# Performance work log

Hardware: AMD Instinct MI355X
Metric: run time of the kernel (lower is better)

## Reference

```python
import jax, jax.numpy as jnp
import numpy as np
import math

B, N, D_FEAT, D_POS, L, H, DK, DV, DM, DI, M = 16, 512, 3, 3, 4, 8, 64, 64, 512, 2048, 64


def _ln(x, g, b, eps=1e-6):
    mu = jnp.mean(x, axis=-1, keepdims=True)
    var = jnp.mean((x - mu) ** 2, axis=-1, keepdims=True)
    return (x - mu) / jnp.sqrt(var + eps) * g + b


def _gelu(x):  # erf-form gelu, matching the torch source exactly
    return x * 0.5 * (1.0 + jax.lax.erf(x / math.sqrt(2.0)))


def setup_inputs() -> dict:
    keys = iter(jax.random.split(jax.random.key(0), 48))
    r = lambda *s: jax.random.normal(next(keys), s, jnp.float32) * 0.02
    inp = {
        'feat_seq': jax.random.normal(next(keys), (B, N, D_FEAT), jnp.float32),
        'r_pos_mat': jax.random.normal(next(keys), (B, N, N, D_POS), jnp.float32),
        'masked_pos': jax.random.randint(next(keys), (B, M), 0, N),
        'fe_w1': r(D_FEAT, DM), 'fe_b1': jnp.zeros((DM,), jnp.float32),
        'fe_w2': r(DM, DM), 'fe_b2': jnp.zeros((DM,), jnp.float32),
        'wq': r(L, DM, H * DK), 'bq': jnp.zeros((L, H * DK), jnp.float32),
        'wk': r(L, DM, H * DK), 'bk': jnp.zeros((L, H * DK), jnp.float32),
        'wv': r(L, DM, H * DV), 'bv': jnp.zeros((L, H * DV), jnp.float32),
        'wp': r(L, D_POS, H, DK), 'bp': jnp.zeros((L, H, DK), jnp.float32),
        'wo': r(L, H * DV, DM), 'bo': jnp.zeros((L, DM), jnp.float32),
        'ln1_g': jnp.ones((L, DM), jnp.float32), 'ln1_b': jnp.zeros((L, DM), jnp.float32),
        'ffn_w1': r(L, DM, DI), 'ffn_b1': jnp.zeros((L, DI), jnp.float32),
        'ffn_w2': r(L, DI, DM), 'ffn_b2': jnp.zeros((L, DM), jnp.float32),
        'ln2_g': jnp.ones((L, DM), jnp.float32), 'ln2_b': jnp.zeros((L, DM), jnp.float32),
        'ln_g': jnp.ones((DM,), jnp.float32), 'ln_b': jnp.zeros((DM,), jnp.float32),
        'lin_w': r(DM, DM), 'lin_b': jnp.zeros((DM,), jnp.float32),
        'dec_w1': r(DM, DM), 'dec_b1': jnp.zeros((DM,), jnp.float32),
        'dec_w2': r(DM, 1), 'dec_b2': jnp.zeros((1,), jnp.float32),
    }
    return inp


def _forward(feat_seq, r_pos_mat, masked_pos, fe_w1, fe_b1, fe_w2, fe_b2,
             wq, bq, wk, bk, wv, bv, wp, bp, wo, bo, ln1_g, ln1_b,
             ffn_w1, ffn_b1, ffn_w2, ffn_b2, ln2_g, ln2_b,
             ln_g, ln_b, lin_w, lin_b, dec_w1, dec_b1, dec_w2, dec_b2):
    b, n, _ = feat_seq.shape
    scale = 1.0 / math.sqrt(DK)  # temperature=None -> sqrt(d_k)
    # TwoLayerFCN feature encoder, non_linear=False (two plain linears)
    x = (feat_seq @ fe_w1 + fe_b1) @ fe_w2 + fe_b2
    x = _ln(x, ln_g, ln_b)  # shared layer_norm (dropout is identity at eval)
    for l in range(L):
        residual = x
        q = (x @ wq[l] + bq[l]).reshape(b, n, H, DK)
        k = (x @ wk[l] + bk[l]).reshape(b, n, H, DK)
        v = (x @ wv[l] + bv[l]).reshape(b, n, H, DV)
        scores = jnp.einsum('bnhk,bmhk->bhnm', q, k)
        # relative-position key r_k[b,n,m,h,k] = r_pos_mat[b,n,m] @ wp + bp
        # rel[b,h,n,m] = q . r_k, computed without materializing [B,N,N,H,DK]
        qw = jnp.einsum('bnhk,phk->bnhp', q, wp[l])
        rel = jnp.einsum('bnhp,bnmp->bhnm', qw, r_pos_mat)
        rel = rel + jnp.einsum('bnhk,hk->bhn', q, bp[l])[..., None]
        attn = jax.nn.softmax((scores + rel) * scale, axis=-1)
        out = jnp.einsum('bhnm,bmhd->bnhd', attn, v).reshape(b, n, H * DV)
        x = _ln(out @ wo[l] + bo[l] + residual, ln1_g[l], ln1_b[l])  # post-norm attn
        x = _ln(jax.nn.relu(x @ ffn_w1[l] + ffn_b1[l]) @ ffn_w2[l] + ffn_b2[l] + x,
                ln2_g[l], ln2_b[l])  # post-norm FFN
    # gather masked positions
    idx = jnp.broadcast_to(masked_pos[:, :, None], (b, masked_pos.shape[1], DM))
    h1 = jnp.take_along_axis(x, idx, axis=1)
    h2 = _ln(_gelu(h1 @ lin_w + lin_b), ln_g, ln_b)  # shared layer_norm params
    dec = (h2 @ dec_w1 + dec_b1) @ dec_w2 + dec_b2  # decoder TwoLayerFCN
    return dec, h1, h2


def reference(feat_seq, r_pos_mat, masked_pos, fe_w1, fe_b1, fe_w2, fe_b2,
              wq, bq, wk, bk, wv, bv, wp, bp, wo, bo, ln1_g, ln1_b,
              ffn_w1, ffn_b1, ffn_w2, ffn_b2, ln2_g, ln2_b,
              ln_g, ln_b, lin_w, lin_b, dec_w1, dec_b1, dec_w2, dec_b2):
    return _forward(feat_seq, r_pos_mat, masked_pos, fe_w1, fe_b1, fe_w2, fe_b2,
                    wq, bq, wk, bk, wv, bv, wp, bp, wo, bo, ln1_g, ln1_b,
                    ffn_w1, ffn_b1, ffn_w2, ffn_b2, ln2_g, ln2_b,
                    ln_g, ln_b, lin_w, lin_b, dec_w1, dec_b1, dec_w2, dec_b2)
```

## Files before the change

### kernel.cpp

```cpp
#include <hip/hip_runtime.h>
#include <hip/hip_bf16.h>
#include <math.h>


using bf16   = __bf16;
using bf16x4 = __attribute__((ext_vector_type(4))) __bf16;
using bf16x8 = __attribute__((ext_vector_type(8))) __bf16;
using f32x4  = __attribute__((ext_vector_type(4))) float;

__device__ __forceinline__ void mfma16(f32x4& d, bf16x8 a, bf16x8 b) {
    asm("v_mfma_f32_16x16x32_bf16 %0, %1, %2, %0" : "+v"(d) : "v"(a), "v"(b));
}

__global__ __launch_bounds__(256) void packb_kernel(
        const float* __restrict__ bq, const float* __restrict__ bk,
        const float* __restrict__ bv, float* __restrict__ out) {
    int i = blockIdx.x * 256 + threadIdx.x;
    if (i >= 6144) return;
    int l = i / 1536, c = i % 1536;
    out[i] = c < 512 ? bq[l * 512 + c] : c < 1024 ? bk[l * 512 + c - 512]
                                                  : bv[l * 512 + c - 1024];
}

__global__ __launch_bounds__(256) void transall_kernel(
        const float* __restrict__ fe_w2, const float* __restrict__ wq,
        const float* __restrict__ wk, const float* __restrict__ wv,
        const float* __restrict__ wo, const float* __restrict__ w1,
        const float* __restrict__ w2, const float* __restrict__ lin_w,
        const float* __restrict__ dec_w1, bf16* __restrict__ dst) {
    __shared__ float t[32][33];
    int id = blockIdx.x;
    const float* src; bf16* d; int K, N, ti;
    if (id < 256)        { src = fe_w2;  d = dst + 12582912; K = 512; N = 512; ti = id; }
    else if (id < 12544) {
        int u = id - 256, l = u / 3072, r = u % 3072;
        bf16* base = dst + (size_t)l * 3145728;
        if      (r < 256)  { src = wq + (size_t)l * 262144;  d = base;           K = 512;  N = 512;  ti = r; }
        else if (r < 512)  { src = wk + (size_t)l * 262144;  d = base + 262144;  K = 512;  N = 512;  ti = r - 256; }
        else if (r < 768)  { src = wv + (size_t)l * 262144;  d = base + 524288;  K = 512;  N = 512;  ti = r - 512; }
        else if (r < 1024) { src = wo + (size_t)l * 262144;  d = base + 786432;  K = 512;  N = 512;  ti = r - 768; }
        else if (r < 2048) { src = w1 + (size_t)l * 1048576; d = base + 1048576; K = 512;  N = 2048; ti = r - 1024; }
        else               { src = w2 + (size_t)l * 1048576; d = base + 2097152; K = 2048; N = 512;  ti = r - 2048; }
    }
    else if (id < 12800) { src = lin_w;  d = dst + 12845056; K = 512; N = 512; ti = id - 12544; }
    else                 { src = dec_w1; d = dst + 13107200; K = 512; N = 512; ti = id - 12800; }
    int nt = N >> 5;
    int n0 = (ti % nt) * 32, k0 = (ti / nt) * 32;
    int tx = threadIdx.x & 31, ty = threadIdx.x >> 5;
#pragma unroll
    for (int i = 0; i < 4; i++)
        t[ty + i * 8][tx] = src[(size_t)(k0 + ty + i * 8) * N + n0 + tx];
    __syncthreads();
#pragma unroll
    for (int i = 0; i < 4; i++)
        d[(size_t)(n0 + ty + i * 8) * K + k0 + tx] = (bf16)t[tx][ty + i * 8];
}

__global__ __launch_bounds__(256) void vt_kernel(
        const bf16* __restrict__ qkv, bf16* __restrict__ vT) {
    __shared__ bf16 t[32][33];
    int s = blockIdx.z;
    int m0 = blockIdx.x * 32, d0 = blockIdx.y * 32;
    int tx = threadIdx.x & 31, ty = threadIdx.x >> 5;
    int b = s >> 3, h = s & 7;
    const bf16* src = qkv + 1024 + (size_t)h * 64;
#pragma unroll
    for (int i = 0; i < 4; i++)
        t[ty + i * 8][tx] = src[(size_t)(b * 512 + m0 + ty + i * 8) * 1536 + d0 + tx];
    __syncthreads();
#pragma unroll
    for (int i = 0; i < 4; i++)
        vT[((size_t)s * 64 + d0 + ty + i * 8) * 512 + m0 + tx] = t[tx][ty + i * 8];
}

__global__ __launch_bounds__(256) void fe1_kernel(
        const float* __restrict__ feat, const float* __restrict__ w1,
        const float* __restrict__ b1, bf16* __restrict__ out) {
    int idx = blockIdx.x * 256 + threadIdx.x;
    int r = idx >> 9, j = idx & 511;
    float f0 = feat[r * 3 + 0], f1 = feat[r * 3 + 1], f2 = feat[r * 3 + 2];
    out[(size_t)r * 512 + j] = (bf16)
        fmaf(f0, w1[j], fmaf(f1, w1[512 + j], fmaf(f2, w1[1024 + j], b1[j])));
}

template<int EPI, bool WF32, bool WB16>
__global__ __launch_bounds__(256) void mm_kernel(
        const bf16* __restrict__ A, const bf16* __restrict__ Bt,
        const float* __restrict__ bias, const float* __restrict__ res,
        float* __restrict__ Cf, bf16* __restrict__ Cb,
        int M, int N, int K) {
    __shared__ bf16 Al[2][8192];
    __shared__ bf16 Bl[2][8192];
    const int tid = threadIdx.x;
    const int lane = tid & 63, wid = tid >> 6;
    const int r0 = blockIdx.y * 128, c0 = blockIdx.x * 128;
    const int wr = (wid >> 1) * 64, wc = (wid & 1) * 64;

    f32x4 acc[4][4] = {};
    const int kTiles = K >> 6;

#define STAGE(buf, kt)                                                                   \
    {                                                                                    \
        const bf16* ga = A + (size_t)r0 * K + (kt) * 64;                                 \
        const bf16* gb = Bt + (size_t)c0 * K + (kt) * 64;                                \
        _Pragma("unroll")                                                                \
        for (int i_ = 0; i_ < 4; i_++) {                                                 \
            int s = tid + i_ * 256;                                                      \
            int row = s >> 3;                                                            \
            int ssl = (s & 7) ^ (row & 7);                                               \
            __builtin_amdgcn_global_load_lds(                                            \
                (const __attribute__((address_space(1))) void*)(ga + (size_t)row * K + ssl * 8), \
                (__attribute__((address_space(3))) void*)(&Al[buf][s * 8]), 16, 0, 0);   \
            __builtin_amdgcn_global_load_lds(                                            \
                (const __attribute__((address_space(1))) void*)(gb + (size_t)row * K + ssl * 8), \
                (__attribute__((address_space(3))) void*)(&Bl[buf][s * 8]), 16, 0, 0);   \
        }                                                                                \
    }

    STAGE(0, 0);
    __syncthreads();

    for (int kt = 0; kt < kTiles; kt++) {
        if (kt + 1 < kTiles) STAGE((kt + 1) & 1, kt + 1);
        const bf16* al = Al[kt & 1];
        const bf16* bl = Bl[kt & 1];
#pragma unroll
        for (int kk = 0; kk < 2; kk++) {
            bf16x8 af[4], bfr[4];
#pragma unroll
            for (int i = 0; i < 4; i++) {
                int arow = wr + i * 16 + (lane & 15);
                int slot = kk * 4 + (lane >> 4);
                af[i] = *(const bf16x8*)(al + arow * 64 + ((slot ^ (arow & 7)) << 3));
                int brow = wc + i * 16 + (lane & 15);
                bfr[i] = *(const bf16x8*)(bl + brow * 64 + ((slot ^ (brow & 7)) << 3));
            }
#pragma unroll
            for (int i = 0; i < 4; i++)
#pragma unroll
                for (int j = 0; j < 4; j++)
                    mfma16(acc[i][j], af[i], bfr[j]);
        }
        __syncthreads();
    }
#undef STAGE

    asm volatile("s_nop 7\n\ts_nop 7");

#pragma unroll
    for (int i = 0; i < 4; i++)
#pragma unroll
        for (int j = 0; j < 4; j++)
#pragma unroll
            for (int q = 0; q < 4; q++) {
                int row = r0 + wr + i * 16 + ((lane >> 4) << 2) + q;
                int col = c0 + wc + j * 16 + (lane & 15);
                float v = acc[i][j][q] + bias[col];
                if (res) v += res[(size_t)row * N + col];
                if (EPI == 1) v = fmaxf(v, 0.f);
                if (EPI == 2) v = 0.5f * v * (1.f + erff(v * 0.7071067811865475f));
                if (WF32) Cf[(size_t)row * N + col] = v;
                if (WB16) Cb[(size_t)row * N + col] = (bf16)v;
            }
}

__global__ __launch_bounds__(256) void ln_kernel(
        const float* __restrict__ in, float* __restrict__ outf, bf16* __restrict__ outb,
        const float* __restrict__ g, const float* __restrict__ b) {
    const int lane = threadIdx.x & 63;
    const size_t row = (size_t)blockIdx.x * 4 + (threadIdx.x >> 6);
    const float* x = in + row * 512;
    float4 a0 = *(const float4*)&x[lane * 4];
    float4 a1 = *(const float4*)&x[256 + lane * 4];
    float s = a0.x + a0.y + a0.z + a0.w + a1.x + a1.y + a1.z + a1.w;
#pragma unroll
    for (int off = 32; off >= 1; off >>= 1) s += __shfl_xor(s, off);
    float mean = s * (1.f / 512.f);
    float d, vs = 0.f;
    d = a0.x - mean; vs += d * d;  d = a0.y - mean; vs += d * d;
    d = a0.z - mean; vs += d * d;  d = a0.w - mean; vs += d * d;
    d = a1.x - mean; vs += d * d;  d = a1.y - mean; vs += d * d;
    d = a1.z - mean; vs += d * d;  d = a1.w - mean; vs += d * d;
#pragma unroll
    for (int off = 32; off >= 1; off >>= 1) vs += __shfl_xor(vs, off);
    float inv = rsqrtf(vs * (1.f / 512.f) + 1e-6f);
    float4 g0 = *(const float4*)&g[lane * 4];
    float4 g1 = *(const float4*)&g[256 + lane * 4];
    float4 b0 = *(const float4*)&b[lane * 4];
    float4 b1v = *(const float4*)&b[256 + lane * 4];
    float o[8];
    o[0] = (a0.x - mean) * inv * g0.x + b0.x;
    o[1] = (a0.y - mean) * inv * g0.y + b0.y;
    o[2] = (a0.z - mean) * inv * g0.z + b0.z;
    o[3] = (a0.w - mean) * inv * g0.w + b0.w;
    o[4] = (a1.x - mean) * inv * g1.x + b1v.x;
    o[5] = (a1.y - mean) * inv * g1.y + b1v.y;
    o[6] = (a1.z - mean) * inv * g1.z + b1v.z;
    o[7] = (a1.w - mean) * inv * g1.w + b1v.w;
    float* y = outf + row * 512;
    *(float4*)&y[lane * 4] = make_float4(o[0], o[1], o[2], o[3]);
    *(float4*)&y[256 + lane * 4] = make_float4(o[4], o[5], o[6], o[7]);
    bf16x4 p0, p1;
#pragma unroll
    for (int i = 0; i < 4; i++) { p0[i] = (bf16)o[i]; p1[i] = (bf16)o[4 + i]; }
    *(bf16x4*)&outb[row * 512 + lane * 4] = p0;
    *(bf16x4*)&outb[row * 512 + 256 + lane * 4] = p1;
}

__global__ __launch_bounds__(256, 2) void attn_kernel(
        const bf16* __restrict__ qb, const bf16* __restrict__ kb,
        const bf16* __restrict__ vT, const float* __restrict__ rpos,
        const float* __restrict__ wp, const float* __restrict__ bp,
        bf16* __restrict__ out) {
    __shared__ bf16 p_lds[4][16][128];
    __shared__ float qw_lds[4][16][4];
    __shared__ bf16 o_lds[4][16][64];
    const int tid = threadIdx.x, lane = tid & 63, wid = tid >> 6;
    const int bh = blockIdx.y, b = bh >> 3, h = bh & 7;
    const int n0 = blockIdx.x * 64 + wid * 16;
    const int lo = lane & 15, hi = lane >> 4;
    const float scale = 0.125f;

    const bf16* qbase = qb + (size_t)(b * 512) * 1536 + h * 64;
    const bf16* kbase = kb + (size_t)(b * 512) * 1536 + h * 64;
    const bf16* vbase = vT + (size_t)bh * 32768;
    const float* rbase = rpos + (size_t)(b * 512 + n0) * 1536;

    {
        int r = lane >> 2, j = lane & 3;
        const float* wvec = (j < 3) ? wp + ((size_t)j * 8 + h) * 64 : bp + (size_t)h * 64;
        const bf16* qr = qbase + (size_t)(n0 + r) * 1536;
        float s = 0.f;
#pragma unroll
        for (int c8 = 0; c8 < 8; c8++) {
            bf16x8 v8 = *(const bf16x8*)(qr + c8 * 8);
#pragma unroll
            for (int i = 0; i < 8; i++) s = fmaf((float)v8[i], wvec[c8 * 8 + i], s);
        }
        qw_lds[wid][r][j] = s;
    }
    bf16x8 af0 = *(const bf16x8*)(qbase + (size_t)(n0 + lo) * 1536 + hi * 8);
    bf16x8 af1 = *(const bf16x8*)(qbase + (size_t)(n0 + lo) * 1536 + 32 + hi * 8);
    __syncthreads();
    float qw[4][4];
#pragma unroll
    for (int q = 0; q < 4; q++)
#pragma unroll
        for (int j = 0; j < 4; j++) qw[q][j] = qw_lds[wid][hi * 4 + q][j];

    f32x4 oacc[4] = {};
    float mrun[4] = {-1e30f, -1e30f, -1e30f, -1e30f};
    float lrun[4] = {0.f, 0.f, 0.f, 0.f};

    for (int mc = 0; mc < 4; mc++) {
        const int m0 = mc * 128;
        f32x4 st[8];
#pragma unroll
        for (int t = 0; t < 8; t++) {
            const bf16* kr = kbase + (size_t)(m0 + t * 16 + lo) * 1536 + hi * 8;
            bf16x8 kf0 = *(const bf16x8*)kr;
            bf16x8 kf1 = *(const bf16x8*)(kr + 32);
            f32x4 z = {};
            mfma16(z, af0, kf0);
            mfma16(z, af1, kf1);
            st[t] = z;
        }
        asm volatile("s_nop 7\n\ts_nop 7");
#pragma unroll
        for (int t = 0; t < 8; t++) {
#pragma unroll
            for (int q = 0; q < 4; q++) {
                const float* rp = rbase + ((size_t)(hi * 4 + q) * 512 + m0 + t * 16 + lo) * 3;
                st[t][q] += fmaf(qw[q][0], rp[0],
                             fmaf(qw[q][1], rp[1], fmaf(qw[q][2], rp[2], qw[q][3])));
            }
        }
        float fac[4];
#pragma unroll
        for (int q = 0; q < 4; q++) {
            float mx = st[0][q];
#pragma unroll
            for (int t = 1; t < 8; t++) mx = fmaxf(mx, st[t][q]);
            mx = fmaxf(mx, __shfl_xor(mx, 1));
            mx = fmaxf(mx, __shfl_xor(mx, 2));
            mx = fmaxf(mx, __shfl_xor(mx, 4));
            mx = fmaxf(mx, __shfl_xor(mx, 8));
            float mnew = fmaxf(mrun[q], mx);
            fac[q] = __expf((mrun[q] - mnew) * scale);
            float ls = 0.f;
#pragma unroll
            for (int t = 0; t < 8; t++) {
                float e = __expf((st[t][q] - mnew) * scale);
                st[t][q] = e;
                ls += e;
            }
            ls += __shfl_xor(ls, 1);
            ls += __shfl_xor(ls, 2);
            ls += __shfl_xor(ls, 4);
            ls += __shfl_xor(ls, 8);
            lrun[q] = lrun[q] * fac[q] + ls;
            mrun[q] = mnew;
        }
#pragma unroll
        for (int dt = 0; dt < 4; dt++) {
            oacc[dt][0] *= fac[0]; oacc[dt][1] *= fac[1];
            oacc[dt][2] *= fac[2]; oacc[dt][3] *= fac[3];
        }
#pragma unroll
        for (int t = 0; t < 8; t++) {
#pragma unroll
            for (int q = 0; q < 4; q++) {
                int rl = hi * 4 + q;
                int c = t * 16 + lo;
                int cs = (((c >> 3) ^ (rl & 7)) << 3) | (c & 7);
                p_lds[wid][rl][cs] = (bf16)st[t][q];
            }
        }
#pragma unroll
        for (int ks = 0; ks < 4; ks++) {
            int chunk = (ks * 4 + hi) ^ (lo & 7);
            bf16x8 pa = *(const bf16x8*)&p_lds[wid][lo][chunk << 3];
#pragma unroll
            for (int dt = 0; dt < 4; dt++) {
                bf16x8 vf = *(const bf16x8*)(vbase + (size_t)(dt * 16 + lo) * 512 + m0 + ks * 32 + hi * 8);
                mfma16(oacc[dt], pa, vf);
            }
        }
    }
    asm volatile("s_nop 7\n\ts_nop 7");
    float inv[4];
#pragma unroll
    for (int q = 0; q < 4; q++) inv[q] = 1.f / lrun[q];
#pragma unroll
    for (int dt = 0; dt < 4; dt++)
#pragma unroll
        for (int q = 0; q < 4; q++)
            o_lds[wid][hi * 4 + q][dt * 16 + lo] = (bf16)(oacc[dt][q] * inv[q]);
    {
        int r = lane >> 2, c = (lane & 3) * 16;
        bf16x8 w0 = *(const bf16x8*)&o_lds[wid][r][c];
        bf16x8 w1 = *(const bf16x8*)&o_lds[wid][r][c + 8];
        bf16* op = out + (size_t)(b * 512 + n0 + r) * 512 + h * 64 + c;
        *(bf16x8*)op = w0;
        *(bf16x8*)(op + 8) = w1;
    }
}

__global__ __launch_bounds__(256) void gather_kernel(
        const float* __restrict__ x, const int* __restrict__ mp,
        float* __restrict__ h1, bf16* __restrict__ h1b) {
    int idx = blockIdx.x * 256 + threadIdx.x;
    int row = idx >> 7, c4 = (idx & 127) * 4;
    int b = row >> 6;
    int src = mp[row];
    float4 v = *(const float4*)&x[((size_t)(b * 512 + src)) * 512 + c4];
    *(float4*)&h1[(size_t)row * 512 + c4] = v;
    bf16x4 p;
    p[0] = (bf16)v.x; p[1] = (bf16)v.y; p[2] = (bf16)v.z; p[3] = (bf16)v.w;
    *(bf16x4*)&h1b[(size_t)row * 512 + c4] = p;
}

__global__ __launch_bounds__(256) void dec2_kernel(
        const float* __restrict__ dmid, const float* __restrict__ w2,
        const float* __restrict__ b2, float* __restrict__ out) {
    const int lane = threadIdx.x & 63;
    const int row = blockIdx.x * 4 + (threadIdx.x >> 6);
    float s = 0.f;
#pragma unroll
    for (int t = 0; t < 8; t++) {
        int c = lane + t * 64;
        s = fmaf(dmid[(size_t)row * 512 + c], w2[c], s);
    }
#pragma unroll
    for (int off = 32; off >= 1; off >>= 1) s += __shfl_xor(s, off);
    if (lane == 0) out[row] = s + b2[0];
}

extern "C" void kernel_launch(void* const* d_in, const int* in_sizes, int n_in,
                              void* d_out, int out_size, void* d_ws, size_t ws_size,
                              hipStream_t stream) {
    const float* feat   = (const float*)d_in[0];
    const float* rpos   = (const float*)d_in[1];
    const int*   mpos   = (const int*)d_in[2];
    const float* fe_w1  = (const float*)d_in[3];
    const float* fe_b1  = (const float*)d_in[4];
    const float* fe_w2  = (const float*)d_in[5];
    const float* fe_b2  = (const float*)d_in[6];
    const float* wq     = (const float*)d_in[7];
    const float* bq     = (const float*)d_in[8];
    const float* wk     = (const float*)d_in[9];
    const float* bk     = (const float*)d_in[10];
    const float* wv     = (const float*)d_in[11];
    const float* bv     = (const float*)d_in[12];
    const float* wp     = (const float*)d_in[13];
    const float* bp     = (const float*)d_in[14];
    const float* wo     = (const float*)d_in[15];
    const float* bo     = (const float*)d_in[16];
    const float* ln1_g  = (const float*)d_in[17];
    const float* ln1_b  = (const float*)d_in[18];
    const float* ffn_w1 = (const float*)d_in[19];
    const float* ffn_b1 = (const float*)d_in[20];
    const float* ffn_w2 = (const float*)d_in[21];
    const float* ffn_b2 = (const float*)d_in[22];
    const float* ln2_g  = (const float*)d_in[23];
    const float* ln2_b  = (const float*)d_in[24];
    const float* ln_g   = (const float*)d_in[25];
    const float* ln_b   = (const float*)d_in[26];
    const float* lin_w  = (const float*)d_in[27];
    const float* lin_b  = (const float*)d_in[28];
    const float* dec_w1 = (const float*)d_in[29];
    const float* dec_b1 = (const float*)d_in[30];
    const float* dec_w2 = (const float*)d_in[31];
    const float* dec_b2 = (const float*)d_in[32];

    char* W = (char*)d_ws;
    float* f_x    = (float*)(W);
    bf16*  qkvb   = (bf16*)(W + 16777216);
    bf16*  tb     = (bf16*)(W + 41943040);
    bf16*  midb   = (bf16*)(W + 16777216);
    bf16*  xb     = (bf16*)(W + 50331648);
    bf16*  vTb    = (bf16*)(W + 58720256);
    bf16*  wTall  = (bf16*)(W + 67108864);
    float* qkbias = (float*)(W + 93847552);
    bf16*  h1b    = tb;
    bf16*  h2b    = tb + 524288;

    bf16* feT  = wTall + 12582912;
    bf16* linT = wTall + 12845056;
    bf16* decT = wTall + 13107200;

    float* outp  = (float*)d_out;
    float* o_dec = outp;
    float* o_h1  = outp + 1024;
    float* o_h2  = outp + 1024 + 524288;

    dim3 g512(4, 64), gQKV(12, 64), gF1(16, 64), gsm(4, 8);

    packb_kernel<<<24, 256, 0, stream>>>(bq, bk, bv, qkbias);
    transall_kernel<<<13056, 256, 0, stream>>>(fe_w2, wq, wk, wv, wo, ffn_w1, ffn_w2,
                                               lin_w, dec_w1, wTall);

    fe1_kernel<<<16384, 256, 0, stream>>>(feat, fe_w1, fe_b1, tb);
    mm_kernel<0, true, false><<<g512, 256, 0, stream>>>(tb, feT, fe_b2, nullptr, f_x, nullptr, 8192, 512, 512);
    ln_kernel<<<2048, 256, 0, stream>>>(f_x, f_x, xb, ln_g, ln_b);

    for (int l = 0; l < 4; l++) {
        bf16* qT  = wTall + (size_t)l * 3145728;
        bf16* oT  = qT + 786432;
        bf16* w1T = qT + 1048576;
        bf16* w2T = qT + 2097152;

        mm_kernel<0, false, true><<<gQKV, 256, 0, stream>>>(xb, qT, qkbias + l * 1536, nullptr, nullptr, qkvb, 8192, 1536, 512);
        vt_kernel<<<dim3(16, 2, 128), 256, 0, stream>>>(qkvb, vTb);
        attn_kernel<<<dim3(8, 128), 256, 0, stream>>>(qkvb, qkvb + 512, vTb, rpos,
                                                      wp + (size_t)l * 1536, bp + (size_t)l * 512, tb);
        mm_kernel<0, true, false><<<g512, 256, 0, stream>>>(tb, oT, bo + l * 512, f_x, f_x, nullptr, 8192, 512, 512);
        ln_kernel<<<2048, 256, 0, stream>>>(f_x, f_x, xb, ln1_g + l * 512, ln1_b + l * 512);
        mm_kernel<1, false, true><<<gF1, 256, 0, stream>>>(xb, w1T, ffn_b1 + l * 2048, nullptr, nullptr, midb, 8192, 2048, 512);
        mm_kernel<0, true, false><<<g512, 256, 0, stream>>>(midb, w2T, ffn_b2 + l * 512, f_x, f_x, nullptr, 8192, 512, 2048);
        ln_kernel<<<2048, 256, 0, stream>>>(f_x, f_x, xb, ln2_g + l * 512, ln2_b + l * 512);
    }

    gather_kernel<<<512, 256, 0, stream>>>(f_x, mpos, o_h1, h1b);
    mm_kernel<2, true, false><<<gsm, 256, 0, stream>>>(h1b, linT, lin_b, nullptr, f_x, nullptr, 1024, 512, 512);
    ln_kernel<<<256, 256, 0, stream>>>(f_x, o_h2, h2b, ln_g, ln_b);
    mm_kernel<0, true, false><<<gsm, 256, 0, stream>>>(h2b, decT, dec_b1, nullptr, f_x, nullptr, 1024, 512, 512);
    dec2_kernel<<<256, 256, 0, stream>>>(f_x, dec_w2, dec_b2, o_dec);
}
```

Baseline: 1.554 ms.

## Pack K per head contiguously and run attention as single-wave blocks

The V-transpose kernel now also copies each head's K slice into a contiguous per-(batch,head) buffer. That buffer reuses the xb region, which is dead after the QKV GEMM. The attention kernel then reads K rows at a 64-element stride instead of the 1536-element interleaved QKV stride, for better locality. Attention is also relaunched as 64-thread, one-wave blocks over 16 query rows, dropping the block barrier and allowing finer scheduling. The cost is an extra K copy per layer and more, smaller blocks.

```diff
diff --git a/kernel.cpp b/kernel.cpp
--- a/kernel.cpp
+++ b/kernel.cpp
@@ -57,16 +57,21 @@
 }
 
 __global__ __launch_bounds__(256) void vt_kernel(
-        const bf16* __restrict__ qkv, bf16* __restrict__ vT) {
+        const bf16* __restrict__ qkv, bf16* __restrict__ vT, bf16* __restrict__ kP) {
     __shared__ bf16 t[32][33];
     int s = blockIdx.z;
     int m0 = blockIdx.x * 32, d0 = blockIdx.y * 32;
     int tx = threadIdx.x & 31, ty = threadIdx.x >> 5;
     int b = s >> 3, h = s & 7;
-    const bf16* src = qkv + 1024 + (size_t)h * 64;
-#pragma unroll
-    for (int i = 0; i < 4; i++)
-        t[ty + i * 8][tx] = src[(size_t)(b * 512 + m0 + ty + i * 8) * 1536 + d0 + tx];
+    const bf16* srcv = qkv + 1024 + (size_t)h * 64;
+    const bf16* srck = qkv + 512 + (size_t)h * 64;
+#pragma unroll
+    for (int i = 0; i < 4; i++) {
+        int m = m0 + ty + i * 8;
+        t[ty + i * 8][tx] = srcv[(size_t)(b * 512 + m) * 1536 + d0 + tx];
+        kP[((size_t)s * 512 + m) * 64 + d0 + tx] =
+            srck[(size_t)(b * 512 + m) * 1536 + d0 + tx];
+    }
     __syncthreads();
 #pragma unroll
     for (int i = 0; i < 4; i++)
@@ -207,22 +212,22 @@
     *(bf16x4*)&outb[row * 512 + 256 + lane * 4] = p1;
 }
 
-__global__ __launch_bounds__(256, 2) void attn_kernel(
-        const bf16* __restrict__ qb, const bf16* __restrict__ kb,
+__global__ __launch_bounds__(64, 4) void attn_kernel(
+        const bf16* __restrict__ qb, const bf16* __restrict__ kP,
         const bf16* __restrict__ vT, const float* __restrict__ rpos,
         const float* __restrict__ wp, const float* __restrict__ bp,
         bf16* __restrict__ out) {
-    __shared__ bf16 p_lds[4][16][128];
-    __shared__ float qw_lds[4][16][4];
-    __shared__ bf16 o_lds[4][16][64];
-    const int tid = threadIdx.x, lane = tid & 63, wid = tid >> 6;
+    __shared__ bf16 p_lds[16][128];
+    __shared__ float qw_lds[16][4];
+    __shared__ bf16 o_lds[16][64];
+    const int lane = threadIdx.x;
     const int bh = blockIdx.y, b = bh >> 3, h = bh & 7;
-    const int n0 = blockIdx.x * 64 + wid * 16;
+    const int n0 = blockIdx.x * 16;
     const int lo = lane & 15, hi = lane >> 4;
     const float scale = 0.125f;
 
     const bf16* qbase = qb + (size_t)(b * 512) * 1536 + h * 64;
-    const bf16* kbase = kb + (size_t)(b * 512) * 1536 + h * 64;
+    const bf16* kbase = kP + (size_t)bh * 32768;
     const bf16* vbase = vT + (size_t)bh * 32768;
     const float* rbase = rpos + (size_t)(b * 512 + n0) * 1536;
 
@@ -237,16 +242,15 @@
 #pragma unroll
             for (int i = 0; i < 8; i++) s = fmaf((float)v8[i], wvec[c8 * 8 + i], s);
         }
-        qw_lds[wid][r][j] = s;
+        qw_lds[r][j] = s;
     }
     bf16x8 af0 = *(const bf16x8*)(qbase + (size_t)(n0 + lo) * 1536 + hi * 8);
     bf16x8 af1 = *(const bf16x8*)(qbase + (size_t)(n0 + lo) * 1536 + 32 + hi * 8);
-    __syncthreads();
     float qw[4][4];
 #pragma unroll
     for (int q = 0; q < 4; q++)
 #pragma unroll
-        for (int j = 0; j < 4; j++) qw[q][j] = qw_lds[wid][hi * 4 + q][j];
+        for (int j = 0; j < 4; j++) qw[q][j] = qw_lds[hi * 4 + q][j];
 
     f32x4 oacc[4] = {};
     float mrun[4] = {-1e30f, -1e30f, -1e30f, -1e30f};
@@ -257,7 +261,7 @@
         f32x4 st[8];
 #pragma unroll
         for (int t = 0; t < 8; t++) {
-            const bf16* kr = kbase + (size_t)(m0 + t * 16 + lo) * 1536 + hi * 8;
+            const bf16* kr = kbase + (size_t)(m0 + t * 16 + lo) * 64 + hi * 8;
             bf16x8 kf0 = *(const bf16x8*)kr;
             bf16x8 kf1 = *(const bf16x8*)(kr + 32);
             f32x4 z = {};
@@ -313,13 +317,13 @@
                 int rl = hi * 4 + q;
                 int c = t * 16 + lo;
                 int cs = (((c >> 3) ^ (rl & 7)) << 3) | (c & 7);
-                p_lds[wid][rl][cs] = (bf16)st[t][q];
+                p_lds[rl][cs] = (bf16)st[t][q];
             }
         }
 #pragma unroll
         for (int ks = 0; ks < 4; ks++) {
             int chunk = (ks * 4 + hi) ^ (lo & 7);
-            bf16x8 pa = *(const bf16x8*)&p_lds[wid][lo][chunk << 3];
+            bf16x8 pa = *(const bf16x8*)&p_lds[lo][chunk << 3];
 #pragma unroll
             for (int dt = 0; dt < 4; dt++) {
                 bf16x8 vf = *(const bf16x8*)(vbase + (size_t)(dt * 16 + lo) * 512 + m0 + ks * 32 + hi * 8);
@@ -335,11 +339,11 @@
     for (int dt = 0; dt < 4; dt++)
 #pragma unroll
         for (int q = 0; q < 4; q++)
-            o_lds[wid][hi * 4 + q][dt * 16 + lo] = (bf16)(oacc[dt][q] * inv[q]);
+            o_lds[hi * 4 + q][dt * 16 + lo] = (bf16)(oacc[dt][q] * inv[q]);
     {
         int r = lane >> 2, c = (lane & 3) * 16;
-        bf16x8 w0 = *(const bf16x8*)&o_lds[wid][r][c];
-        bf16x8 w1 = *(const bf16x8*)&o_lds[wid][r][c + 8];
+        bf16x8 w0 = *(const bf16x8*)&o_lds[r][c];
+        bf16x8 w1 = *(const bf16x8*)&o_lds[r][c + 8];
         bf16* op = out + (size_t)(b * 512 + n0 + r) * 512 + h * 64 + c;
         *(bf16x8*)op = w0;
         *(bf16x8*)(op + 8) = w1;
@@ -419,6 +423,7 @@
     bf16*  tb     = (bf16*)(W + 41943040);
     bf16*  midb   = (bf16*)(W + 16777216);
     bf16*  xb     = (bf16*)(W + 50331648);
+    bf16*  kPb    = (bf16*)(W + 50331648);
     bf16*  vTb    = (bf16*)(W + 58720256);
     bf16*  wTall  = (bf16*)(W + 67108864);
     float* qkbias = (float*)(W + 93847552);
@@ -451,8 +456,8 @@
         bf16* w2T = qT + 2097152;
 
         mm_kernel<0, false, true><<<gQKV, 256, 0, stream>>>(xb, qT, qkbias + l * 1536, nullptr, nullptr, qkvb, 8192, 1536, 512);
-        vt_kernel<<<dim3(16, 2, 128), 256, 0, stream>>>(qkvb, vTb);
-        attn_kernel<<<dim3(8, 128), 256, 0, stream>>>(qkvb, qkvb + 512, vTb, rpos,
+        vt_kernel<<<dim3(16, 2, 128), 256, 0, stream>>>(qkvb, vTb, kPb);
+        attn_kernel<<<dim3(32, 128), 64, 0, stream>>>(qkvb, kPb, vTb, rpos,
                                                       wp + (size_t)l * 1536, bp + (size_t)l * 512, tb);
         mm_kernel<0, true, false><<<g512, 256, 0, stream>>>(tb, oT, bo + l * 512, f_x, f_x, nullptr, 8192, 512, 512);
         ln_kernel<<<2048, 256, 0, stream>>>(f_x, f_x, xb, ln1_g + l * 512, ln1_b + l * 512);
```

New measurement: 1.576 ms. Within noise of the previous version (+1.4%).
